# Kernel tuning notes

Measured on AMD Instinct MI355X. Metric: run time of the kernel, lower is better.

Reference implementation:

```python
import jax, jax.numpy as jnp
import numpy as np

N, E = 100000, 3200000
F_IN, H, ED, C = 21, 64, 3, 2
EPS = 1e-5


def setup_inputs() -> dict:
    key = jax.random.key(0)
    ks = jax.random.split(key, 20)
    def lin(k, fan_out, fan_in):
        s = 1.0 / np.sqrt(fan_in)
        return jax.random.uniform(k, (fan_out, fan_in), jnp.float32, -s, s)
    inp = {
        'x': jax.random.normal(ks[0], (N, F_IN), jnp.float32),
        'edge_index': jax.random.randint(ks[1], (2, E), 0, N, jnp.int64),
        'edge_attr': jax.random.normal(ks[2], (E, ED), jnp.float32),
        # edge encoder Linear(ED -> H)
        'We': lin(ks[3], H, ED), 'be': jnp.zeros((H,), jnp.float32),
        # conv1 SAGEConv(F_IN -> H): lin_l (neighbors, with bias), lin_r (root, no bias)
        'W1l': lin(ks[4], H, F_IN), 'b1l': jnp.zeros((H,), jnp.float32),
        'W1r': lin(ks[5], H, F_IN),
        # conv2 SAGEConv(H -> H)
        'W2l': lin(ks[6], H, H), 'b2l': jnp.zeros((H,), jnp.float32),
        'W2r': lin(ks[7], H, H),
        # BatchNorms
        'g1': jnp.ones((H,), jnp.float32), 'beta1': jnp.zeros((H,), jnp.float32),
        'g2': jnp.ones((H,), jnp.float32), 'beta2': jnp.zeros((H,), jnp.float32),
        # classifier Linear(H -> C)
        'Wc': lin(ks[8], C, H), 'bc': jnp.zeros((C,), jnp.float32),
    }
    return inp


def _bn(h, g, b):
    # training-mode BatchNorm1d: batch stats, biased variance
    mu = jnp.mean(h, axis=0)
    var = jnp.mean(jnp.square(h - mu), axis=0)
    return (h - mu) * jax.lax.rsqrt(var + EPS) * g + b


def reference(x, edge_index, edge_attr, We, be, W1l, b1l, W1r, W2l, b2l, W2r,
              g1, beta1, g2, beta2, Wc, bc):
    n = x.shape[0]
    src, dst = edge_index[0], edge_index[1]
    # degree (in-degree at target), clamped to 1 for mean aggregation
    deg = jax.ops.segment_sum(jnp.ones((src.shape[0],), x.dtype), dst, num_segments=n)
    inv_deg = (1.0 / jnp.maximum(deg, 1.0))[:, None]  # [N,1]

    def sage(h, Wl, bl, Wr):
        agg = jax.ops.segment_sum(h[src], dst, num_segments=n) * inv_deg  # mean over in-neighbors
        return agg @ Wl.T + bl + h @ Wr.T

    # edge feature encoding + scatter-add to target nodes
    edge_enc = jax.nn.relu(edge_attr @ We.T + be)                # [E,H]
    edge_agg = jax.ops.segment_sum(edge_enc, dst, num_segments=n)  # [N,H]

    h = sage(x, W1l, b1l, W1r) + edge_agg
    h = jax.nn.relu(_bn(h, g1, beta1))
    # dropout omitted (deterministic reference)
    h = sage(h, W2l, b2l, W2r)
    h = jax.nn.relu(_bn(h, g2, beta2))
    return h @ Wc.T + bc  # logits [N,2]
```

## Files before the change

### kernel.cpp

```cpp
#include <hip/hip_runtime.h>
#include <hip/hip_fp16.h>

#define NN 100000
#define NE 3200000
#define F_IN 21
#define HID 64
#define EPS 1e-5f

#define NB 1000
#define BN 100
#define SCAP 3712
#define AB 256
#define AEPB 12500


__global__ void __launch_bounds__(256) kC1_slab_r15(
    const int* __restrict__ src, const int* __restrict__ dst,
    const float* __restrict__ eattr,
    int* __restrict__ segStart, int* __restrict__ btot,
    float4* __restrict__ packB, unsigned char* __restrict__ dlArr) {
    __shared__ int lcnt[NB];
    __shared__ int lpart[256];
    __shared__ int lcur[NB];
    int tid = threadIdx.x;
    for (int i = tid; i < NB; i += 256) lcnt[i] = 0;
    __syncthreads();
    int base = blockIdx.x * AEPB;
    for (int k = tid; k < AEPB; k += 256) atomicAdd(&lcnt[dst[base + k] / BN], 1);
    __syncthreads();
    int mySum = 0;
    if (tid < 250)
        mySum = lcnt[4 * tid] + lcnt[4 * tid + 1] + lcnt[4 * tid + 2] + lcnt[4 * tid + 3];
    lpart[tid] = mySum;
    __syncthreads();
    for (int off = 1; off < 256; off <<= 1) {
        int v = (tid >= off) ? lpart[tid - off] : 0;
        __syncthreads();
        lpart[tid] += v;
        __syncthreads();
    }
    if (tid < 250) {
        int run = lpart[tid] - mySum;
#pragma unroll
        for (int j = 0; j < 4; ++j) {
            int b = 4 * tid + j;
            int c = lcnt[b];
            int st = base + run;
            lcur[b] = st;
            segStart[b * AB + blockIdx.x] = st;
            if (c) atomicAdd(&btot[b], c);
            run += c;
        }
    }
    if (tid == 0) segStart[NB * AB + blockIdx.x] = base + AEPB;
    __syncthreads();
    for (int k = tid; k < AEPB; k += 256) {
        int e = base + k;
        int d = dst[e];
        int b = d / BN;
        int dl = d - b * BN;
        int pos = atomicAdd(&lcur[b], 1);
        size_t eb = (size_t)e * 3;
        float4 pk = {__int_as_float(src[e] | (dl << 17)),
                     eattr[eb], eattr[eb + 1], eattr[eb + 2]};
        packB[pos] = pk;
        dlArr[pos] = (unsigned char)dl;
    }
}

__global__ void kB2_scan_r15(const int* __restrict__ btot, int* __restrict__ bucketBase,
                             int* __restrict__ rowptr) {
    __shared__ int lds[1024];
    int t = threadIdx.x;
    int v = (t < NB) ? btot[t] : 0;
    lds[t] = v;
    __syncthreads();
    for (int off = 1; off < 1024; off <<= 1) {
        int u = (t >= off) ? lds[t - off] : 0;
        __syncthreads();
        lds[t] += u;
        __syncthreads();
    }
    if (t < NB) bucketBase[t] = lds[t] - v;
    if (t == 0) rowptr[NN] = NE;
}

__global__ void kP_pad_r15(const float* __restrict__ x, __half* __restrict__ xh) {
    int i = blockIdx.x * blockDim.x + threadIdx.x;
    int st = gridDim.x * blockDim.x;
    for (; i < NN * 32; i += st) {
        int n = i >> 5, c = i & 31;
        xh[i] = __float2half((c < F_IN) ? x[(size_t)n * F_IN + c] : 0.f);
    }
}


#define R3X(v) { v += __shfl_xor(v, 8); v += __shfl_xor(v, 16); v += __shfl_xor(v, 32); }
#define R2X(v) { v += __shfl_xor(v, 16); v += __shfl_xor(v, 32); }
#define PICK(v, kk) ((kk) == 0 ? (v).x : (kk) == 1 ? (v).y : (kk) == 2 ? (v).z : (v).w)

__global__ void __launch_bounds__(512) kFuse_r15(
    const float4* __restrict__ packB, const unsigned char* __restrict__ dlArr,
    const int* __restrict__ segStart, const int* __restrict__ bucketBase,
    const __half* __restrict__ xh, const float* __restrict__ x,
    const float* __restrict__ We, const float* __restrict__ be,
    const float* __restrict__ W1l, const float* __restrict__ b1l,
    const float* __restrict__ W1r,
    float* __restrict__ H1, int* __restrict__ csr_src, int* __restrict__ rowptr,
    float* __restrict__ gsum, float* __restrict__ gsq) {
    __shared__ uint2 stageU[SCAP];
    __shared__ unsigned short stageB[SCAP];
    __shared__ int segA[AB], segL[AB];
    __shared__ int lcnt2[BN], lofs[BN], lcur2[BN];
    __shared__ float eLds[8 * HID];
    __shared__ float bs[HID], bq[HID];
    int tid = threadIdx.x;
    int b = blockIdx.x;
    int base = bucketBase[b];
    if (tid < AB) {
        int a = segStart[b * AB + tid];
        segA[tid] = a;
        segL[tid] = segStart[(b + 1) * AB + tid] - a;
    }
    for (int i = tid; i < BN; i += 512) lcnt2[i] = 0;
    if (tid < HID) { bs[tid] = 0.f; bq[tid] = 0.f; }
    __syncthreads();
    int lane = tid & 63, wid = tid >> 6;
    for (int s = wid; s < AB; s += 8) {
        int L = segL[s], A = segA[s];
        for (int i = lane; i < L; i += 64) atomicAdd(&lcnt2[dlArr[A + i]], 1);
    }
    __syncthreads();
    if (tid == 0) {
        int run = 0;
        for (int d = 0; d < BN; ++d) { lofs[d] = run; lcur2[d] = run; run += lcnt2[d]; }
    }
    __syncthreads();
    if (tid < BN) rowptr[b * BN + tid] = base + lofs[tid];
    for (int s = wid; s < AB; s += 8) {
        int L = segL[s], A = segA[s];
        for (int i = lane; i < L; i += 64) {
            float4 pk = packB[A + i];
            int enc = __float_as_int(pk.x);
            int dl = enc >> 17;
            int pos = atomicAdd(&lcur2[dl], 1);
            if (pos < SCAP) {
                __half2 h01 = __floats2half2_rn(pk.y, pk.z);
                uint2 u = {(unsigned int)enc, *(unsigned int*)&h01};
                stageU[pos] = u;
                stageB[pos] = __half_as_ushort(__float2half(pk.w));
            }
        }
    }
    __syncthreads();
    int cntB = lofs[BN - 1] + lcnt2[BN - 1];
    int lim = min(cntB, SCAP);
    for (int i = tid; i < lim; i += 512)
        csr_src[base + i] = (int)(stageU[i].x & 0x1FFFF);
    int g = lane >> 3, q = lane & 7;
    float w0[8], w1[8], w2[8], bqv[8];
#pragma unroll
    for (int r = 0; r < 8; ++r) {
        int ch = 8 * q + r;
        w0[r] = We[ch * 3]; w1[r] = We[ch * 3 + 1]; w2[r] = We[ch * 3 + 2];
        bqv[r] = be[ch];
    }
    float wl[F_IN], wr[F_IN];
#pragma unroll
    for (int k = 0; k < F_IN; ++k) {
        wl[k] = W1l[lane * F_IN + k];
        wr[k] = W1r[lane * F_IN + k];
    }
    float b1 = b1l[lane];
    float psum = 0.f, psq = 0.f;
    for (int d = wid; d < BN; d += 8) {
        int lbeg = lofs[d];
        int deg = lcnt2[d];
        int lend = lbeg + deg;
        float aX0 = 0, aX1 = 0, aX2 = 0, aX3 = 0;
        float aE[8] = {0, 0, 0, 0, 0, 0, 0, 0};
        for (int i0 = lbeg + g; i0 < lend; i0 += 32) {
            uint2 xv[4];
            uint2 su[4];
            float a2f[4];
            float mk[4];
#pragma unroll
            for (int u = 0; u < 4; ++u) {
                int i = i0 + u * 8;
                mk[u] = (i < lend) ? 1.f : 0.f;
                int ic = min(min(i, lend - 1), SCAP - 1);
                su[u] = stageU[ic];
                a2f[u] = __half2float(__ushort_as_half(stageB[ic]));
                int s = (int)(su[u].x & 0x1FFFF);
                xv[u] = *(const uint2*)(xh + (size_t)s * 32 + 4 * q);
            }
#pragma unroll
            for (int u = 0; u < 4; ++u) {
                float2 f0 = __half22float2(*(__half2*)&xv[u].x);
                float2 f1 = __half22float2(*(__half2*)&xv[u].y);
                float2 a01 = __half22float2(*(__half2*)&su[u].y);
                float m = mk[u];
                aX0 = fmaf(f0.x, m, aX0);
                aX1 = fmaf(f0.y, m, aX1);
                aX2 = fmaf(f1.x, m, aX2);
                aX3 = fmaf(f1.y, m, aX3);
#pragma unroll
                for (int r = 0; r < 8; ++r) {
                    float e = fmaf(w0[r], a01.x,
                              fmaf(w1[r], a01.y, fmaf(w2[r], a2f[u], bqv[r])));
                    aE[r] = fmaf(fmaxf(e, 0.f), m, aE[r]);
                }
            }
        }
        R3X(aX0) R3X(aX1) R3X(aX2) R3X(aX3)
#pragma unroll
        for (int r = 0; r < 8; ++r) { R3X(aE[r]) }
        if (g == 0) {
            float4 e0 = {aE[0], aE[1], aE[2], aE[3]};
            float4 e1 = {aE[4], aE[5], aE[6], aE[7]};
            *(float4*)(eLds + wid * HID + 8 * q) = e0;
            *(float4*)(eLds + wid * HID + 8 * q + 4) = e1;
        }
        int n = b * BN + d;
        float4 aXq = {aX0, aX1, aX2, aX3};
        float xv = (lane < F_IN) ? x[(size_t)n * F_IN + lane] : 0.f;
        float own = b1, agg = 0.f;
#pragma unroll
        for (int k = 0; k < F_IN; ++k) {
            own = fmaf(wr[k], __shfl(xv, k), own);
            agg = fmaf(wl[k], __shfl(PICK(aXq, k & 3), k >> 2), agg);
        }
        float invd = 1.f / fmaxf((float)deg, 1.f);
        float h = own + agg * invd + eLds[wid * HID + lane];
        H1[(size_t)n * HID + lane] = h;
        psum += h; psq += h * h;
    }
    atomicAdd(&bs[lane], psum);
    atomicAdd(&bq[lane], psq);
    __syncthreads();
    if (tid < HID) {
        atomicAdd(&gsum[tid], bs[tid]);
        atomicAdd(&gsq[tid], bq[tid]);
    }
}

__global__ void kActB_r15(const float* __restrict__ H1,
                          const float* __restrict__ gsum, const float* __restrict__ gsq,
                          const float* __restrict__ g1, const float* __restrict__ beta1,
                          __half* __restrict__ act) {
    __shared__ float sc[HID], sh[HID];
    int t = threadIdx.x;
    if (t < HID) {
        float mu = gsum[t] * (1.f / (float)NN);
        float var = gsq[t] * (1.f / (float)NN) - mu * mu;
        float s = rsqrtf(var + EPS) * g1[t];
        sc[t] = s;
        sh[t] = beta1[t] - mu * s;
    }
    __syncthreads();
    int i = blockIdx.x * blockDim.x + t;
    int st = gridDim.x * blockDim.x;
    for (; i < NN * HID; i += st) {
        int c = i & 63;
        act[i] = __float2half(fmaxf(fmaf(H1[i], sc[c], sh[c]), 0.f));
    }
}


__global__ void __launch_bounds__(256, 2) kG2f_r15(
    const __half* __restrict__ act, const int* __restrict__ csr_src,
    const int* __restrict__ rowptr,
    const float* __restrict__ W2l, const float* __restrict__ W2r,
    const float* __restrict__ b2l,
    float* __restrict__ h2, float* __restrict__ gsum, float* __restrict__ gsq) {
    __shared__ float ldsL[HID * HID];
    __shared__ float ldsR[HID * HID];
    __shared__ float bs[HID], bq[HID];
    for (int i = threadIdx.x; i < HID * HID; i += blockDim.x) {
        int k = i >> 6, c = i & 63;
        ldsL[i] = W2l[c * HID + k];
        ldsR[i] = W2r[c * HID + k];
    }
    if (threadIdx.x < HID) { bs[threadIdx.x] = 0.f; bq[threadIdx.x] = 0.f; }
    __syncthreads();
    int lane = threadIdx.x & 63;
    int g = lane >> 4, c4 = lane & 15;
    float b2 = b2l[lane];
    int gw = blockIdx.x * 4 + (threadIdx.x >> 6);
    int nw = gridDim.x * 4;
    float psum = 0.f, psq = 0.f;
    for (int n = gw; n < NN; n += nw) {
        int beg = rowptr[n], end = rowptr[n + 1];
        int deg = end - beg;
        float a0 = 0, a1 = 0, a2 = 0, a3 = 0;
        for (int p0 = beg; p0 < end; p0 += 64) {
            int cnt = min(64, end - p0);
            int sL = (lane < cnt) ? csr_src[p0 + lane] : 0;
            int jm = (cnt + 3) >> 2;
            for (int jb = 0; jb < jm; jb += 8) {
                uint2 v[8];
                float mk[8];
#pragma unroll
                for (int u = 0; u < 8; ++u) {
                    int idx = (jb + u) * 4 + g;
                    int s = __shfl(sL, idx);
                    mk[u] = (idx < cnt) ? 1.f : 0.f;
                    v[u] = *(const uint2*)(act + (size_t)s * HID + 4 * c4);
                }
#pragma unroll
                for (int u = 0; u < 8; ++u) {
                    float2 f0 = __half22float2(*(__half2*)&v[u].x);
                    float2 f1 = __half22float2(*(__half2*)&v[u].y);
                    float m = mk[u];
                    a0 = fmaf(f0.x, m, a0);
                    a1 = fmaf(f0.y, m, a1);
                    a2 = fmaf(f1.x, m, a2);
                    a3 = fmaf(f1.y, m, a3);
                }
            }
        }
        R2X(a0) R2X(a1) R2X(a2) R2X(a3)
        float invd = 1.f / fmaxf((float)deg, 1.f);
        float4 aq = {a0 * invd, a1 * invd, a2 * invd, a3 * invd};
        float v2 = __half2float(act[(size_t)n * HID + lane]);
        float o0 = b2, o1 = 0.f, o2 = 0.f, o3 = 0.f;
#pragma unroll
        for (int k = 0; k < HID; k += 4) {
            float va0 = __shfl(PICK(aq, k & 3), k >> 2);
            float vb0 = __shfl(v2, k);
            o0 = fmaf(ldsL[k * HID + lane], va0, fmaf(ldsR[k * HID + lane], vb0, o0));
            float va1 = __shfl(PICK(aq, (k + 1) & 3), (k + 1) >> 2);
            float vb1 = __shfl(v2, k + 1);
            o1 = fmaf(ldsL[(k + 1) * HID + lane], va1, fmaf(ldsR[(k + 1) * HID + lane], vb1, o1));
            float va2 = __shfl(PICK(aq, (k + 2) & 3), (k + 2) >> 2);
            float vb2 = __shfl(v2, k + 2);
            o2 = fmaf(ldsL[(k + 2) * HID + lane], va2, fmaf(ldsR[(k + 2) * HID + lane], vb2, o2));
            float va3 = __shfl(PICK(aq, (k + 3) & 3), (k + 3) >> 2);
            float vb3 = __shfl(v2, k + 3);
            o3 = fmaf(ldsL[(k + 3) * HID + lane], va3, fmaf(ldsR[(k + 3) * HID + lane], vb3, o3));
        }
        float o = (o0 + o1) + (o2 + o3);
        h2[(size_t)n * HID + lane] = o;
        psum += o; psq += o * o;
    }
    atomicAdd(&bs[lane], psum);
    atomicAdd(&bq[lane], psq);
    __syncthreads();
    if (threadIdx.x < HID) {
        atomicAdd(&gsum[threadIdx.x], bs[threadIdx.x]);
        atomicAdd(&gsq[threadIdx.x], bq[threadIdx.x]);
    }
}


__global__ void kJ_out_r15(const float* __restrict__ H2,
                           const float* __restrict__ gsum, const float* __restrict__ gsq,
                           const float* __restrict__ g2, const float* __restrict__ beta2,
                           const float* __restrict__ Wc, const float* __restrict__ bc,
                           float* __restrict__ out) {
    __shared__ float scL[HID], shL[HID];
    int t = threadIdx.x;
    if (t < HID) {
        float mu = gsum[t] * (1.f / (float)NN);
        float var = gsq[t] * (1.f / (float)NN) - mu * mu;
        float s = rsqrtf(var + EPS) * g2[t];
        scL[t] = s;
        shL[t] = beta2[t] - mu * s;
    }
    __syncthreads();
    int lane = t & 63;
    int g = lane >> 4, c4 = lane & 15;
    int wv = blockIdx.x * 4 + (t >> 6);
    int nw = gridDim.x * 4;
    float4 sc = *(const float4*)(scL + 4 * c4);
    float4 sh = *(const float4*)(shL + 4 * c4);
    float4 w0 = *(const float4*)(Wc + 4 * c4);
    float4 w1 = *(const float4*)(Wc + HID + 4 * c4);
    float b0 = bc[0], b1 = bc[1];
    for (int tt = wv; tt < NN / 4; tt += nw) {
        int n = tt * 4 + g;
        float4 h = *(const float4*)(H2 + (size_t)n * HID + 4 * c4);
        float vx = fmaxf(fmaf(h.x, sc.x, sh.x), 0.f);
        float vy = fmaxf(fmaf(h.y, sc.y, sh.y), 0.f);
        float vz = fmaxf(fmaf(h.z, sc.z, sh.z), 0.f);
        float vw = fmaxf(fmaf(h.w, sc.w, sh.w), 0.f);
        float r0 = vx * w0.x + vy * w0.y + vz * w0.z + vw * w0.w;
        float r1 = vx * w1.x + vy * w1.y + vz * w1.z + vw * w1.w;
#pragma unroll
        for (int off = 1; off <= 8; off <<= 1) {
            r0 += __shfl_xor(r0, off);
            r1 += __shfl_xor(r1, off);
        }
        if (c4 == 0) {
            out[(size_t)n * 2] = r0 + b0;
            out[(size_t)n * 2 + 1] = r1 + b1;
        }
    }
}


extern "C" void kernel_launch(void* const* d_in, const int* in_sizes, int n_in,
                              void* d_out, int out_size, void* d_ws, size_t ws_size,
                              hipStream_t stream) {
    const float* x = (const float*)d_in[0];
    const int* ei = (const int*)d_in[1];
    const float* eattr = (const float*)d_in[2];
    const float* We = (const float*)d_in[3];
    const float* be = (const float*)d_in[4];
    const float* W1l = (const float*)d_in[5];
    const float* b1l = (const float*)d_in[6];
    const float* W1r = (const float*)d_in[7];
    const float* W2l = (const float*)d_in[8];
    const float* b2l = (const float*)d_in[9];
    const float* W2r = (const float*)d_in[10];
    const float* g1 = (const float*)d_in[11];
    const float* beta1 = (const float*)d_in[12];
    const float* g2 = (const float*)d_in[13];
    const float* beta2 = (const float*)d_in[14];
    const float* Wc = (const float*)d_in[15];
    const float* bc = (const float*)d_in[16];
    float* out = (float*)d_out;

    const int* e_src = ei;
    const int* e_dst = ei + NE;

    char* ws = (char*)d_ws;
    size_t off = 0;
    auto alloc = [&](size_t b) {
        char* p = ws + off;
        off += (b + 255) & ~(size_t)255;
        return p;
    };
    int* rowptr = (int*)alloc((NN + 1) * sizeof(int));
    int* segStart = (int*)alloc((size_t)(NB + 1) * AB * sizeof(int));
    int* btot = (int*)alloc(NB * sizeof(int));
    int* bucketBase = (int*)alloc(NB * sizeof(int));
    float4* packB = (float4*)alloc((size_t)NE * 16);
    unsigned char* dlArr = (unsigned char*)alloc((size_t)NE);
    int* csr_src = (int*)alloc((size_t)NE * sizeof(int));
    __half* xh = (__half*)alloc((size_t)NN * 32 * sizeof(__half));
    float* H1 = (float*)alloc((size_t)NN * HID * sizeof(float));
    __half* act = (__half*)alloc((size_t)NN * HID * sizeof(__half));
    float* stats = (float*)alloc(256 * sizeof(float));
    float* gsum1 = stats, *gsq1 = stats + 64, *gsum2 = stats + 128, *gsq2 = stats + 192;

    float* h2 = (float*)packB;

    hipMemsetAsync(btot, 0, NB * sizeof(int), stream);
    hipMemsetAsync(stats, 0, 256 * sizeof(float), stream);

    kC1_slab_r15<<<AB, 256, 0, stream>>>(e_src, e_dst, eattr, segStart, btot, packB, dlArr);
    kB2_scan_r15<<<1, 1024, 0, stream>>>(btot, bucketBase, rowptr);
    kP_pad_r15<<<1024, 256, 0, stream>>>(x, xh);
    kFuse_r15<<<NB, 512, 0, stream>>>(packB, dlArr, segStart, bucketBase,
                                      xh, x, We, be, W1l, b1l, W1r,
                                      H1, csr_src, rowptr, gsum1, gsq1);
    kActB_r15<<<2048, 256, 0, stream>>>(H1, gsum1, gsq1, g1, beta1, act);
    kG2f_r15<<<4096, 256, 0, stream>>>(act, csr_src, rowptr, W2l, W2r, b2l,
                                       h2, gsum2, gsq2);
    kJ_out_r15<<<512, 256, 0, stream>>>(h2, gsum2, gsq2, g2, beta2, Wc, bc, out);
}
```

Before: 604.9 us.

## Split edge bucketing into histogram, global scan and placement for contiguous buckets

```diff
diff --git a/kernel.cpp b/kernel.cpp
--- a/kernel.cpp
+++ b/kernel.cpp
@@ -14,46 +14,56 @@
 #define AEPB 12500
 
 
-__global__ void __launch_bounds__(256) kC1_slab_r15(
+__global__ void __launch_bounds__(256) kH_hist_r17(
+    const int* __restrict__ dst, int* __restrict__ hist ) {
+    __shared__ int lcnt[NB];
+    int tid = threadIdx.x;
+    for (int i = tid; i < NB; i += 256) lcnt[i] = 0;
+    __syncthreads();
+    int base = blockIdx.x * AEPB;
+    for (int k = tid; k < AEPB; k += 256) atomicAdd(&lcnt[dst[base + k] / BN], 1);
+    __syncthreads();
+    for (int i = tid; i < NB; i += 256) hist[blockIdx.x * NB + i] = lcnt[i];
+}
+
+
+__global__ void kB2_scan_r17(const int* __restrict__ hist,
+                             int* __restrict__ segOfs, int* __restrict__ bucketBase,
+                             int* __restrict__ rowptr) {
+    __shared__ int lds[1024];
+    int t = threadIdx.x;
+    int tot = 0;
+    if (t < NB)
+        for (int blk = 0; blk < AB; ++blk) tot += hist[blk * NB + t];
+    lds[t] = tot;
+    __syncthreads();
+    for (int off = 1; off < 1024; off <<= 1) {
+        int u = (t >= off) ? lds[t - off] : 0;
+        __syncthreads();
+        lds[t] += u;
+        __syncthreads();
+    }
+    if (t < NB) {
+        int run = lds[t] - tot;
+        bucketBase[t] = run;
+        for (int blk = 0; blk < AB; ++blk) {
+            segOfs[blk * NB + t] = run;
+            run += hist[blk * NB + t];
+        }
+    }
+    if (t == 0) rowptr[NN] = NE;
+}
+
+
+__global__ void __launch_bounds__(256) kC1_place_r17(
     const int* __restrict__ src, const int* __restrict__ dst,
-    const float* __restrict__ eattr,
-    int* __restrict__ segStart, int* __restrict__ btot,
+    const float* __restrict__ eattr, const int* __restrict__ segOfs,
     float4* __restrict__ packB, unsigned char* __restrict__ dlArr) {
-    __shared__ int lcnt[NB];
-    __shared__ int lpart[256];
     __shared__ int lcur[NB];
     int tid = threadIdx.x;
-    for (int i = tid; i < NB; i += 256) lcnt[i] = 0;
+    for (int i = tid; i < NB; i += 256) lcur[i] = segOfs[blockIdx.x * NB + i];
     __syncthreads();
     int base = blockIdx.x * AEPB;
-    for (int k = tid; k < AEPB; k += 256) atomicAdd(&lcnt[dst[base + k] / BN], 1);
-    __syncthreads();
-    int mySum = 0;
-    if (tid < 250)
-        mySum = lcnt[4 * tid] + lcnt[4 * tid + 1] + lcnt[4 * tid + 2] + lcnt[4 * tid + 3];
-    lpart[tid] = mySum;
-    __syncthreads();
-    for (int off = 1; off < 256; off <<= 1) {
-        int v = (tid >= off) ? lpart[tid - off] : 0;
-        __syncthreads();
-        lpart[tid] += v;
-        __syncthreads();
-    }
-    if (tid < 250) {
-        int run = lpart[tid] - mySum;
-#pragma unroll
-        for (int j = 0; j < 4; ++j) {
-            int b = 4 * tid + j;
-            int c = lcnt[b];
-            int st = base + run;
-            lcur[b] = st;
-            segStart[b * AB + blockIdx.x] = st;
-            if (c) atomicAdd(&btot[b], c);
-            run += c;
-        }
-    }
-    if (tid == 0) segStart[NB * AB + blockIdx.x] = base + AEPB;
-    __syncthreads();
     for (int k = tid; k < AEPB; k += 256) {
         int e = base + k;
         int d = dst[e];
@@ -68,24 +78,7 @@
     }
 }
 
-__global__ void kB2_scan_r15(const int* __restrict__ btot, int* __restrict__ bucketBase,
-                             int* __restrict__ rowptr) {
-    __shared__ int lds[1024];
-    int t = threadIdx.x;
-    int v = (t < NB) ? btot[t] : 0;
-    lds[t] = v;
-    __syncthreads();
-    for (int off = 1; off < 1024; off <<= 1) {
-        int u = (t >= off) ? lds[t - off] : 0;
-        __syncthreads();
-        lds[t] += u;
-        __syncthreads();
-    }
-    if (t < NB) bucketBase[t] = lds[t] - v;
-    if (t == 0) rowptr[NN] = NE;
-}
-
-__global__ void kP_pad_r15(const float* __restrict__ x, __half* __restrict__ xh) {
+__global__ void kP_pad_r17(const float* __restrict__ x, __half* __restrict__ xh) {
     int i = blockIdx.x * blockDim.x + threadIdx.x;
     int st = gridDim.x * blockDim.x;
     for (; i < NN * 32; i += st) {
@@ -99,9 +92,9 @@
 #define R2X(v) { v += __shfl_xor(v, 16); v += __shfl_xor(v, 32); }
 #define PICK(v, kk) ((kk) == 0 ? (v).x : (kk) == 1 ? (v).y : (kk) == 2 ? (v).z : (v).w)
 
-__global__ void __launch_bounds__(512) kFuse_r15(
+__global__ void __launch_bounds__(512) kFuse_r17(
     const float4* __restrict__ packB, const unsigned char* __restrict__ dlArr,
-    const int* __restrict__ segStart, const int* __restrict__ bucketBase,
+    const int* __restrict__ bucketBase,
     const __half* __restrict__ xh, const float* __restrict__ x,
     const float* __restrict__ We, const float* __restrict__ be,
     const float* __restrict__ W1l, const float* __restrict__ b1l,
@@ -110,53 +103,53 @@
     float* __restrict__ gsum, float* __restrict__ gsq) {
     __shared__ uint2 stageU[SCAP];
     __shared__ unsigned short stageB[SCAP];
-    __shared__ int segA[AB], segL[AB];
     __shared__ int lcnt2[BN], lofs[BN], lcur2[BN];
+    __shared__ int scanT[128];
     __shared__ float eLds[8 * HID];
     __shared__ float bs[HID], bq[HID];
     int tid = threadIdx.x;
     int b = blockIdx.x;
     int base = bucketBase[b];
-    if (tid < AB) {
-        int a = segStart[b * AB + tid];
-        segA[tid] = a;
-        segL[tid] = segStart[(b + 1) * AB + tid] - a;
-    }
+    int bend = (b == NB - 1) ? NE : bucketBase[b + 1];
+    int cntB = bend - base;
     for (int i = tid; i < BN; i += 512) lcnt2[i] = 0;
     if (tid < HID) { bs[tid] = 0.f; bq[tid] = 0.f; }
     __syncthreads();
-    int lane = tid & 63, wid = tid >> 6;
-    for (int s = wid; s < AB; s += 8) {
-        int L = segL[s], A = segA[s];
-        for (int i = lane; i < L; i += 64) atomicAdd(&lcnt2[dlArr[A + i]], 1);
-    }
-    __syncthreads();
-    if (tid == 0) {
-        int run = 0;
-        for (int d = 0; d < BN; ++d) { lofs[d] = run; lcur2[d] = run; run += lcnt2[d]; }
-    }
-    __syncthreads();
-    if (tid < BN) rowptr[b * BN + tid] = base + lofs[tid];
-    for (int s = wid; s < AB; s += 8) {
-        int L = segL[s], A = segA[s];
-        for (int i = lane; i < L; i += 64) {
-            float4 pk = packB[A + i];
-            int enc = __float_as_int(pk.x);
-            int dl = enc >> 17;
-            int pos = atomicAdd(&lcur2[dl], 1);
-            if (pos < SCAP) {
-                __half2 h01 = __floats2half2_rn(pk.y, pk.z);
-                uint2 u = {(unsigned int)enc, *(unsigned int*)&h01};
-                stageU[pos] = u;
-                stageB[pos] = __half_as_ushort(__float2half(pk.w));
-            }
-        }
-    }
-    __syncthreads();
-    int cntB = lofs[BN - 1] + lcnt2[BN - 1];
+    for (int i = tid; i < cntB; i += 512) atomicAdd(&lcnt2[dlArr[base + i]], 1);
+    __syncthreads();
+    if (tid < 128) scanT[tid] = (tid < BN) ? lcnt2[tid] : 0;
+    __syncthreads();
+    for (int off = 1; off < 128; off <<= 1) {
+        int v = 0;
+        if (tid < 128 && tid >= off) v = scanT[tid - off];
+        __syncthreads();
+        if (tid < 128) scanT[tid] += v;
+        __syncthreads();
+    }
+    if (tid < BN) {
+        int ex = scanT[tid] - lcnt2[tid];
+        lofs[tid] = ex;
+        lcur2[tid] = ex;
+        rowptr[b * BN + tid] = base + ex;
+    }
+    __syncthreads();
+    for (int i = tid; i < cntB; i += 512) {
+        float4 pk = packB[base + i];
+        int enc = __float_as_int(pk.x);
+        int dl = enc >> 17;
+        int pos = atomicAdd(&lcur2[dl], 1);
+        if (pos < SCAP) {
+            __half2 h01 = __floats2half2_rn(pk.y, pk.z);
+            uint2 u = {(unsigned int)enc, *(unsigned int*)&h01};
+            stageU[pos] = u;
+            stageB[pos] = __half_as_ushort(__float2half(pk.w));
+        }
+    }
+    __syncthreads();
     int lim = min(cntB, SCAP);
     for (int i = tid; i < lim; i += 512)
         csr_src[base + i] = (int)(stageU[i].x & 0x1FFFF);
+    int lane = tid & 63, wid = tid >> 6;
     int g = lane >> 3, q = lane & 7;
     float w0[8], w1[8], w2[8], bqv[8];
 #pragma unroll
@@ -244,7 +237,7 @@
     }
 }
 
-__global__ void kActB_r15(const float* __restrict__ H1,
+__global__ void kActB_r17(const float* __restrict__ H1,
                           const float* __restrict__ gsum, const float* __restrict__ gsq,
                           const float* __restrict__ g1, const float* __restrict__ beta1,
                           __half* __restrict__ act) {
@@ -267,7 +260,7 @@
 }
 
 
-__global__ void __launch_bounds__(256, 2) kG2f_r15(
+__global__ void __launch_bounds__(256, 2) kG2f_r17(
     const __half* __restrict__ act, const int* __restrict__ csr_src,
     const int* __restrict__ rowptr,
     const float* __restrict__ W2l, const float* __restrict__ W2r,
@@ -353,7 +346,7 @@
 }
 
 
-__global__ void kJ_out_r15(const float* __restrict__ H2,
+__global__ void kJ_out_r17(const float* __restrict__ H2,
                            const float* __restrict__ gsum, const float* __restrict__ gsq,
                            const float* __restrict__ g2, const float* __restrict__ beta2,
                            const float* __restrict__ Wc, const float* __restrict__ bc,
@@ -432,8 +425,8 @@
         return p;
     };
     int* rowptr = (int*)alloc((NN + 1) * sizeof(int));
-    int* segStart = (int*)alloc((size_t)(NB + 1) * AB * sizeof(int));
-    int* btot = (int*)alloc(NB * sizeof(int));
+    int* hist = (int*)alloc((size_t)AB * NB * sizeof(int));
+    int* segOfs = (int*)alloc((size_t)AB * NB * sizeof(int));
     int* bucketBase = (int*)alloc(NB * sizeof(int));
     float4* packB = (float4*)alloc((size_t)NE * 16);
     unsigned char* dlArr = (unsigned char*)alloc((size_t)NE);
@@ -446,17 +439,17 @@
 
     float* h2 = (float*)packB;
 
-    hipMemsetAsync(btot, 0, NB * sizeof(int), stream);
     hipMemsetAsync(stats, 0, 256 * sizeof(float), stream);
 
-    kC1_slab_r15<<<AB, 256, 0, stream>>>(e_src, e_dst, eattr, segStart, btot, packB, dlArr);
-    kB2_scan_r15<<<1, 1024, 0, stream>>>(btot, bucketBase, rowptr);
-    kP_pad_r15<<<1024, 256, 0, stream>>>(x, xh);
-    kFuse_r15<<<NB, 512, 0, stream>>>(packB, dlArr, segStart, bucketBase,
-                                      xh, x, We, be, W1l, b1l, W1r,
+    kH_hist_r17<<<AB, 256, 0, stream>>>(e_dst, hist);
+    kB2_scan_r17<<<1, 1024, 0, stream>>>(hist, segOfs, bucketBase, rowptr);
+    kP_pad_r17<<<1024, 256, 0, stream>>>(x, xh);
+    kC1_place_r17<<<AB, 256, 0, stream>>>(e_src, e_dst, eattr, segOfs, packB, dlArr);
+    kFuse_r17<<<NB, 512, 0, stream>>>(packB, dlArr, bucketBase, xh, x,
+                                      We, be, W1l, b1l, W1r,
                                       H1, csr_src, rowptr, gsum1, gsq1);
-    kActB_r15<<<2048, 256, 0, stream>>>(H1, gsum1, gsq1, g1, beta1, act);
-    kG2f_r15<<<4096, 256, 0, stream>>>(act, csr_src, rowptr, W2l, W2r, b2l,
+    kActB_r17<<<2048, 256, 0, stream>>>(H1, gsum1, gsq1, g1, beta1, act);
+    kG2f_r17<<<2048, 256, 0, stream>>>(act, csr_src, rowptr, W2l, W2r, b2l,
                                        h2, gsum2, gsq2);
-    kJ_out_r15<<<512, 256, 0, stream>>>(h2, gsum2, gsq2, g2, beta2, Wc, bc, out);
-}
+    kJ_out_r17<<<512, 256, 0, stream>>>(h2, gsum2, gsq2, g2, beta2, Wc, bc, out);
+}
```

Measured after the change: 525.7 us. -13.1%, faster.
